# Optimization experiments

Measured on AMD Instinct MI355X. Metric: run time of the kernel, lower is better.

## Reference

```python
import jax, jax.numpy as jnp
import numpy as np

IN_F, OUT_F, RANK = 4096, 4096, 16
ALPHA = 32.0
SCALING = ALPHA / RANK


def setup_inputs() -> dict:
    key = jax.random.key(0)
    kx, kw, ka, kb = jax.random.split(key, 4)
    x = jax.random.normal(kx, (4, 2048, IN_F), dtype=jnp.float32)
    # base linear weight [out, in] (kaiming-uniform-like scale)
    bound_w = 1.0 / np.sqrt(IN_F)
    W = jax.random.uniform(kw, (OUT_F, IN_F), minval=-bound_w, maxval=bound_w, dtype=jnp.float32)
    # lora_A [rank, in]: kaiming uniform; lora_B [out, rank]: nonzero for testing
    bound_a = np.sqrt(6.0 / IN_F) / np.sqrt(1.0 + 5.0)
    lora_A = jax.random.uniform(ka, (RANK, IN_F), minval=-bound_a, maxval=bound_a, dtype=jnp.float32)
    lora_B = jax.random.normal(kb, (OUT_F, RANK), dtype=jnp.float32) * 0.02
    return {"x": x, "W": W, "lora_A": lora_A, "lora_B": lora_B}


def reference(x, W, lora_A, lora_B):
    # base: x @ W^T  -> [b, s, out]
    base = jnp.einsum("bsi,oi->bso", x, W)
    # low-rank path: (x @ A^T) @ B^T * scaling (dropout p=0 -> identity)
    r = jnp.einsum("bsi,ri->bsr", x, lora_A)  # [b, s, rank]
    lora = jnp.einsum("bsr,or->bso", r, lora_B) * SCALING
    return base + lora
```

## Files before the change

kernel.cpp:

```cpp
#include <hip/hip_runtime.h>
#include <stdint.h>
#include <stddef.h>

#define IN_F    4096
#define OUT_F   4096
#define MTOK    8192
#define RANK    16
#define SCALING 2.0f

typedef __attribute__((ext_vector_type(8))) short          bf16x8;
typedef __attribute__((ext_vector_type(4))) float          f32x4;
typedef __attribute__((ext_vector_type(4))) float          fl4;
typedef __attribute__((ext_vector_type(4))) unsigned short u16x4;
typedef __attribute__((ext_vector_type(8))) unsigned short u16x8;

static __device__ __forceinline__ unsigned short f2bf(float f) {
  union { float f; uint32_t u; } v; v.f = f;
  return (unsigned short)((v.u + 0x7fffu + ((v.u >> 16) & 1u)) >> 16);
}

static __device__ __forceinline__ void gload16(const void* g, void* l) {
  __builtin_amdgcn_global_load_lds(
      (const __attribute__((address_space(1))) uint32_t*)g,
      (__attribute__((address_space(3))) uint32_t*)l,
      16, 0, 0);
}

__global__ void merge_w_kernel(const float* __restrict__ W,
                               const float* __restrict__ lA,
                               const float* __restrict__ lB,
                               unsigned short* __restrict__ Weff) {
  __shared__ float Bs[RANK];
  const int o = blockIdx.x;
  if (threadIdx.x < RANK) Bs[threadIdx.x] = lB[o * RANK + threadIdx.x] * SCALING;
  __syncthreads();
  for (int c = threadIdx.x * 4; c < IN_F; c += 256 * 4) {
    fl4 w = *(const fl4*)(W + (size_t)o * IN_F + c);
#pragma unroll
    for (int r = 0; r < RANK; ++r) {
      const float b = Bs[r];
      const fl4 a = *(const fl4*)(lA + (size_t)r * IN_F + c);
      w[0] += b * a[0]; w[1] += b * a[1]; w[2] += b * a[2]; w[3] += b * a[3];
    }
    u16x4 p;
    p[0] = f2bf(w[0]); p[1] = f2bf(w[1]); p[2] = f2bf(w[2]); p[3] = f2bf(w[3]);
    *(u16x4*)(Weff + (size_t)o * IN_F + c) = p;
  }
}

__global__ void conv_x_kernel(const float* __restrict__ x,
                              unsigned short* __restrict__ xb) {
  const size_t i = ((size_t)blockIdx.x * 256 + threadIdx.x) * 8;
  const fl4 a = *(const fl4*)(x + i);
  const fl4 b = *(const fl4*)(x + i + 4);
  u16x8 p;
  p[0] = f2bf(a[0]); p[1] = f2bf(a[1]); p[2] = f2bf(a[2]); p[3] = f2bf(a[3]);
  p[4] = f2bf(b[0]); p[5] = f2bf(b[1]); p[6] = f2bf(b[2]); p[7] = f2bf(b[3]);
  *(u16x8*)(xb + i) = p;
}

__global__ __launch_bounds__(512, 2) void gemm8p_kernel(
    const unsigned short* __restrict__ X,
    const unsigned short* __restrict__ Wf,
    float* __restrict__ Out) {
  __shared__ char lds[131072];
  const int tid  = threadIdx.x;
  const int lane = tid & 63;
  const int wave = tid >> 6;
  const int wr = wave >> 2;
  const int wc = wave & 3;
  const int fr = lane & 15;
  const int fq = lane >> 4;

  const int bid = blockIdx.x;
  const int swz = (bid & 7) * 64 + (bid >> 3);
  const int tm = swz & 31;
  const int tn = swz >> 5;
  const int m0 = tm << 8;
  const int n0 = tn << 8;

  const unsigned short* Ag = X  + (size_t)m0 * IN_F;
  const unsigned short* Bg = Wf + (size_t)n0 * IN_F;

  const int rIW = lane >> 3;
  const int csw = ((lane & 7) ^ rIW) << 3;

  const int aBase = wr * 16384 + fr * 128;
  const int bBase = 65536 + (wc >> 1) * 16384 + (wc & 1) * 8192 + fr * 128;
  const int cA0 = (fq << 4) ^ ((fr & 7) << 4);
  const int cA1 = cA0 ^ 64;

#define STAGE(OP, H, BUF, K) do {                                              \
    const unsigned short* _g = (OP) ? Bg : Ag;                                 \
    const int _r0 = (H) * 128 + wave * 16 + rIW;                               \
    char* _d = lds + (OP) * 65536 + (BUF) * 32768 + (H) * 16384 +              \
               wave * 2048 + (lane << 4);                                      \
    gload16(_g + (size_t)_r0 * IN_F + (K) + csw, _d);                          \
    gload16(_g + (size_t)(_r0 + 8) * IN_F + (K) + csw, _d + 1024);             \
  } while (0)

#define LDA(BUF, M, KK) (*(const bf16x8*)(lds + (BUF) * 32768 + aBase + (M) * 2048 + (KK)))
#define LDB(BUF, N, KK) (*(const bf16x8*)(lds + (BUF) * 32768 + bBase + (N) * 2048 + (KK)))

  f32x4 acc[8][4];
#pragma unroll
  for (int i = 0; i < 8; ++i)
#pragma unroll
    for (int j = 0; j < 4; ++j) acc[i][j] = (f32x4){0.f, 0.f, 0.f, 0.f};

  bf16x8 a[8], b0[4], b1[4];

  STAGE(0, 0, 0, 0); STAGE(0, 1, 0, 0); STAGE(1, 0, 0, 0); STAGE(1, 1, 0, 0);

  for (int t = 0; t < 64; ++t) {
    const int b  = t & 1;
    const int nb = b ^ 1;
    const int kn = (t + 1) << 6;
    const bool pf = (t + 1 < 64);

    if (pf) {
      STAGE(0, 0, nb, kn);
      asm volatile("s_waitcnt vmcnt(2)" ::: "memory");
    } else {
      asm volatile("s_waitcnt vmcnt(0)" ::: "memory");
    }
    __builtin_amdgcn_s_barrier();
#pragma unroll
    for (int mi = 0; mi < 4; ++mi) { a[mi*2] = LDA(b, mi, cA0); a[mi*2+1] = LDA(b, mi, cA1); }
#pragma unroll
    for (int ni = 0; ni < 2; ++ni) { b0[ni*2] = LDB(b, ni, cA0); b0[ni*2+1] = LDB(b, ni, cA1); }
    asm volatile("s_waitcnt lgkmcnt(0)" ::: "memory");
    __builtin_amdgcn_s_setprio(1);
#pragma unroll
    for (int mi = 0; mi < 4; ++mi)
#pragma unroll
      for (int ni = 0; ni < 2; ++ni) {
        acc[mi][ni] = __builtin_amdgcn_mfma_f32_16x16x32_bf16(a[mi*2],   b0[ni*2],   acc[mi][ni], 0, 0, 0);
        acc[mi][ni] = __builtin_amdgcn_mfma_f32_16x16x32_bf16(a[mi*2+1], b0[ni*2+1], acc[mi][ni], 0, 0, 0);
      }
    __builtin_amdgcn_s_setprio(0);
    __builtin_amdgcn_s_barrier();

    if (pf) STAGE(0, 1, nb, kn);
    __builtin_amdgcn_s_barrier();
#pragma unroll
    for (int ni = 0; ni < 2; ++ni) { b1[ni*2] = LDB(b, 2+ni, cA0); b1[ni*2+1] = LDB(b, 2+ni, cA1); }
    asm volatile("s_waitcnt lgkmcnt(0)" ::: "memory");
    __builtin_amdgcn_s_setprio(1);
#pragma unroll
    for (int mi = 0; mi < 4; ++mi)
#pragma unroll
      for (int ni = 0; ni < 2; ++ni) {
        acc[mi][2+ni] = __builtin_amdgcn_mfma_f32_16x16x32_bf16(a[mi*2],   b1[ni*2],   acc[mi][2+ni], 0, 0, 0);
        acc[mi][2+ni] = __builtin_amdgcn_mfma_f32_16x16x32_bf16(a[mi*2+1], b1[ni*2+1], acc[mi][2+ni], 0, 0, 0);
      }
    __builtin_amdgcn_s_setprio(0);
    __builtin_amdgcn_s_barrier();

    if (pf) STAGE(1, 0, nb, kn);
    __builtin_amdgcn_s_barrier();
#pragma unroll
    for (int mi = 0; mi < 4; ++mi) { a[mi*2] = LDA(b, 4+mi, cA0); a[mi*2+1] = LDA(b, 4+mi, cA1); }
    asm volatile("s_waitcnt lgkmcnt(0)" ::: "memory");
    __builtin_amdgcn_s_setprio(1);
#pragma unroll
    for (int mi = 0; mi < 4; ++mi)
#pragma unroll
      for (int ni = 0; ni < 2; ++ni) {
        acc[4+mi][2+ni] = __builtin_amdgcn_mfma_f32_16x16x32_bf16(a[mi*2],   b1[ni*2],   acc[4+mi][2+ni], 0, 0, 0);
        acc[4+mi][2+ni] = __builtin_amdgcn_mfma_f32_16x16x32_bf16(a[mi*2+1], b1[ni*2+1], acc[4+mi][2+ni], 0, 0, 0);
      }
    __builtin_amdgcn_s_setprio(0);
    __builtin_amdgcn_s_barrier();

    if (pf) STAGE(1, 1, nb, kn);
    __builtin_amdgcn_s_barrier();
#pragma unroll
    for (int ni = 0; ni < 2; ++ni) { b0[ni*2] = LDB(b, ni, cA0); b0[ni*2+1] = LDB(b, ni, cA1); }
    asm volatile("s_waitcnt lgkmcnt(0)" ::: "memory");
    __builtin_amdgcn_s_setprio(1);
#pragma unroll
    for (int mi = 0; mi < 4; ++mi)
#pragma unroll
      for (int ni = 0; ni < 2; ++ni) {
        acc[4+mi][ni] = __builtin_amdgcn_mfma_f32_16x16x32_bf16(a[mi*2],   b0[ni*2],   acc[4+mi][ni], 0, 0, 0);
        acc[4+mi][ni] = __builtin_amdgcn_mfma_f32_16x16x32_bf16(a[mi*2+1], b0[ni*2+1], acc[4+mi][ni], 0, 0, 0);
      }
    __builtin_amdgcn_s_setprio(0);
    __builtin_amdgcn_s_barrier();
  }

#pragma unroll
  for (int mi = 0; mi < 8; ++mi) {
    const int row0 = m0 + wr * 128 + mi * 16 + fq * 4;
#pragma unroll
    for (int ni = 0; ni < 4; ++ni) {
      const int col = n0 + wc * 64 + ni * 16 + fr;
#pragma unroll
      for (int j = 0; j < 4; ++j)
        Out[(size_t)(row0 + j) * OUT_F + col] = acc[mi][ni][j];
    }
  }
#undef STAGE
#undef LDA
#undef LDB
}

__global__ __launch_bounds__(256) void gemm_f32x_kernel(
    const float* __restrict__ X,
    const unsigned short* __restrict__ Weff,
    float* __restrict__ Out) {
  __shared__ unsigned short As[128][32];
  __shared__ unsigned short Bs[128][32];

  const int tid  = threadIdx.x;
  const int lane = tid & 63;
  const int wave = tid >> 6;
  const int wr = wave >> 1, wc = wave & 1;
  const int fr = lane & 15, fq = lane >> 4;

  const int bid = blockIdx.x;
  const int m0 = (bid & 63) * 128;
  const int n0 = (bid >> 6) * 128;

  f32x4 acc[4][4];
#pragma unroll
  for (int i = 0; i < 4; ++i)
#pragma unroll
    for (int j = 0; j < 4; ++j) acc[i][j] = (f32x4){0.f, 0.f, 0.f, 0.f};

  const int srow = tid >> 2;
  const int sseg = tid & 3;

  for (int k0 = 0; k0 < IN_F; k0 += 32) {
    if (k0) __syncthreads();
    {
      const unsigned short* gB = Weff + (size_t)(n0 + srow) * IN_F + k0 + sseg * 8;
      gload16(gB, &Bs[srow][sseg * 8]);
      gload16(gB + (size_t)64 * IN_F, &Bs[64 + srow][sseg * 8]);
    }
#pragma unroll
    for (int it = 0; it < 4; ++it) {
      const int c   = tid + it * 256;
      const int row = c >> 3;
      const int c4  = (c & 7) * 4;
      const fl4 v = *(const fl4*)(X + (size_t)(m0 + row) * IN_F + k0 + c4);
      u16x4 p;
      p[0] = f2bf(v[0]); p[1] = f2bf(v[1]); p[2] = f2bf(v[2]); p[3] = f2bf(v[3]);
      *(u16x4*)&As[row][c4] = p;
    }
    __syncthreads();

    bf16x8 af[4], bfm[4];
#pragma unroll
    for (int m = 0; m < 4; ++m)
      af[m] = *(const bf16x8*)&As[wr * 64 + m * 16 + fr][fq * 8];
#pragma unroll
    for (int n = 0; n < 4; ++n)
      bfm[n] = *(const bf16x8*)&Bs[wc * 64 + n * 16 + fr][fq * 8];
#pragma unroll
    for (int m = 0; m < 4; ++m)
#pragma unroll
      for (int n = 0; n < 4; ++n)
        acc[m][n] = __builtin_amdgcn_mfma_f32_16x16x32_bf16(af[m], bfm[n], acc[m][n], 0, 0, 0);
  }

#pragma unroll
  for (int m = 0; m < 4; ++m) {
    const int row0 = m0 + wr * 64 + m * 16 + fq * 4;
#pragma unroll
    for (int n = 0; n < 4; ++n) {
      const int col = n0 + wc * 64 + n * 16 + fr;
#pragma unroll
      for (int j = 0; j < 4; ++j)
        Out[(size_t)(row0 + j) * OUT_F + col] = acc[m][n][j];
    }
  }
}

__global__ void lora_r_kernel(const float* __restrict__ x,
                              const float* __restrict__ lA,
                              float* __restrict__ r) {
  const int idx = blockIdx.x * 256 + threadIdx.x;
  const int m = idx / RANK, rr = idx % RANK;
  float acc = 0.f;
  for (int k = 0; k < IN_F; ++k)
    acc += x[(size_t)m * IN_F + k] * lA[(size_t)rr * IN_F + k];
  r[idx] = acc * SCALING;
}

__global__ void naive_out_kernel(const float* __restrict__ x,
                                 const float* __restrict__ W,
                                 const float* __restrict__ lB,
                                 const float* __restrict__ r,
                                 float* __restrict__ out) {
  const size_t idx = (size_t)blockIdx.x * 256 + threadIdx.x;
  const int m = (int)(idx / OUT_F), n = (int)(idx % OUT_F);
  float acc = 0.f;
  for (int k = 0; k < IN_F; ++k)
    acc += x[(size_t)m * IN_F + k] * W[(size_t)n * IN_F + k];
#pragma unroll
  for (int rr = 0; rr < RANK; ++rr)
    acc += r[(size_t)m * RANK + rr] * lB[(size_t)n * RANK + rr];
  out[idx] = acc;
}

extern "C" void kernel_launch(void* const* d_in, const int* in_sizes, int n_in,
                              void* d_out, int out_size, void* d_ws, size_t ws_size,
                              hipStream_t stream) {
  const float* x  = (const float*)d_in[0];
  const float* W  = (const float*)d_in[1];
  const float* lA = (const float*)d_in[2];
  const float* lB = (const float*)d_in[3];
  float* out = (float*)d_out;

  const size_t weff_bytes = (size_t)OUT_F * IN_F * 2;
  const size_t xb_bytes   = (size_t)MTOK * IN_F * 2;

  if (ws_size >= weff_bytes + xb_bytes) {
    unsigned short* Weff = (unsigned short*)d_ws;
    unsigned short* xb   = (unsigned short*)((char*)d_ws + weff_bytes);
    merge_w_kernel<<<OUT_F, 256, 0, stream>>>(W, lA, lB, Weff);
    conv_x_kernel<<<(MTOK * (size_t)IN_F) / (256 * 8), 256, 0, stream>>>(x, xb);
    gemm8p_kernel<<<(MTOK / 256) * (OUT_F / 256), 512, 0, stream>>>(xb, Weff, out);
  } else if (ws_size >= weff_bytes) {
    unsigned short* Weff = (unsigned short*)d_ws;
    merge_w_kernel<<<OUT_F, 256, 0, stream>>>(W, lA, lB, Weff);
    gemm_f32x_kernel<<<(MTOK / 128) * (OUT_F / 128), 256, 0, stream>>>(x, Weff, out);
  } else {
    float* r = (float*)d_ws;
    lora_r_kernel<<<(MTOK * RANK) / 256, 256, 0, stream>>>(x, lA, r);
    naive_out_kernel<<<(size_t)MTOK * OUT_F / 256, 256, 0, stream>>>(x, W, lB, r, out);
  }
}
```

Measured before the change: 364.0 us.

## Reorder staged loads so B tile lands first and overlap LDS reads with MFMA phases

Splits the global-to-LDS staging into separate A and B chunk macros and reorders the prefetch so B chunks are issued first and A chunks last. The vmcnt waits are relaxed to match. LDS fragment reads for the next MFMA phase are now issued before the barrier that follows the current phase, and the explicit lgkmcnt(0) waits are removed, so LDS reads overlap with MFMA execution. The intent is to cut barrier and wait stalls in the 256x256 bf16 GEMM main loop. The risk is that correctness now depends on the reworked wait counts, the buffer lifetimes and compiler-inserted lgkm waits.

```diff
diff --git a/kernel.cpp b/kernel.cpp
--- a/kernel.cpp
+++ b/kernel.cpp
@@ -90,13 +90,23 @@
   const int cA0 = (fq << 4) ^ ((fr & 7) << 4);
   const int cA1 = cA0 ^ 64;
 
-#define STAGE(OP, H, BUF, K) do {                                              \
-    const unsigned short* _g = (OP) ? Bg : Ag;                                 \
-    const int _r0 = (H) * 128 + wave * 16 + rIW;                               \
-    char* _d = lds + (OP) * 65536 + (BUF) * 32768 + (H) * 16384 +              \
-               wave * 2048 + (lane << 4);                                      \
-    gload16(_g + (size_t)_r0 * IN_F + (K) + csw, _d);                          \
-    gload16(_g + (size_t)(_r0 + 8) * IN_F + (K) + csw, _d + 1024);             \
+#define STAGE_A(C, BUF, K) do {                                                \
+    const int _rh = (C) * 64 + (wave & 3) * 16;                                \
+    const int _r0 = (wave >> 2) * 128 + _rh + rIW;                             \
+    char* _d = lds + (BUF) * 32768 + (wave >> 2) * 16384 + _rh * 128 +         \
+               (lane << 4);                                                    \
+    gload16(Ag + (size_t)_r0 * IN_F + (K) + csw, _d);                          \
+    gload16(Ag + (size_t)(_r0 + 8) * IN_F + (K) + csw, _d + 1024);             \
+  } while (0)
+
+#define STAGE_B(C, BUF, K) do {                                                \
+    const int _s  = wave >> 1;                                                 \
+    const int _rh = (_s & 1) * 64 + (C) * 32 + (wave & 1) * 16;                \
+    const int _r0 = (_s >> 1) * 128 + _rh + rIW;                               \
+    char* _d = lds + 65536 + (BUF) * 32768 + (_s >> 1) * 16384 + _rh * 128 +   \
+               (lane << 4);                                                    \
+    gload16(Bg + (size_t)_r0 * IN_F + (K) + csw, _d);                          \
+    gload16(Bg + (size_t)(_r0 + 8) * IN_F + (K) + csw, _d + 1024);             \
   } while (0)
 
 #define LDA(BUF, M, KK) (*(const bf16x8*)(lds + (BUF) * 32768 + aBase + (M) * 2048 + (KK)))
@@ -110,26 +120,25 @@
 
   bf16x8 a[8], b0[4], b1[4];
 
-  STAGE(0, 0, 0, 0); STAGE(0, 1, 0, 0); STAGE(1, 0, 0, 0); STAGE(1, 1, 0, 0);
+  STAGE_B(0, 0, 0); STAGE_B(1, 0, 0); STAGE_A(0, 0, 0); STAGE_A(1, 0, 0);
 
   for (int t = 0; t < 64; ++t) {
-    const int b  = t & 1;
-    const int nb = b ^ 1;
+    const int bu = t & 1;
+    const int nb = bu ^ 1;
     const int kn = (t + 1) << 6;
     const bool pf = (t + 1 < 64);
 
     if (pf) {
-      STAGE(0, 0, nb, kn);
+      STAGE_B(0, nb, kn);
+      asm volatile("s_waitcnt vmcnt(4)" ::: "memory");
+    } else {
       asm volatile("s_waitcnt vmcnt(2)" ::: "memory");
-    } else {
-      asm volatile("s_waitcnt vmcnt(0)" ::: "memory");
-    }
-    __builtin_amdgcn_s_barrier();
-#pragma unroll
-    for (int mi = 0; mi < 4; ++mi) { a[mi*2] = LDA(b, mi, cA0); a[mi*2+1] = LDA(b, mi, cA1); }
-#pragma unroll
-    for (int ni = 0; ni < 2; ++ni) { b0[ni*2] = LDB(b, ni, cA0); b0[ni*2+1] = LDB(b, ni, cA1); }
-    asm volatile("s_waitcnt lgkmcnt(0)" ::: "memory");
+    }
+    __builtin_amdgcn_s_barrier();
+#pragma unroll
+    for (int mi = 0; mi < 4; ++mi) { a[mi*2] = LDA(bu, mi, cA0); a[mi*2+1] = LDA(bu, mi, cA1); }
+#pragma unroll
+    for (int ni = 0; ni < 2; ++ni) { b0[ni*2] = LDB(bu, ni, cA0); b0[ni*2+1] = LDB(bu, ni, cA1); }
     __builtin_amdgcn_s_setprio(1);
 #pragma unroll
     for (int mi = 0; mi < 4; ++mi)
@@ -139,13 +148,17 @@
         acc[mi][ni] = __builtin_amdgcn_mfma_f32_16x16x32_bf16(a[mi*2+1], b0[ni*2+1], acc[mi][ni], 0, 0, 0);
       }
     __builtin_amdgcn_s_setprio(0);
-    __builtin_amdgcn_s_barrier();
-
-    if (pf) STAGE(0, 1, nb, kn);
-    __builtin_amdgcn_s_barrier();
-#pragma unroll
-    for (int ni = 0; ni < 2; ++ni) { b1[ni*2] = LDB(b, 2+ni, cA0); b1[ni*2+1] = LDB(b, 2+ni, cA1); }
-    asm volatile("s_waitcnt lgkmcnt(0)" ::: "memory");
+#pragma unroll
+    for (int ni = 0; ni < 2; ++ni) { b1[ni*2] = LDB(bu, 2+ni, cA0); b1[ni*2+1] = LDB(bu, 2+ni, cA1); }
+    __builtin_amdgcn_s_barrier();
+
+    if (pf) {
+      STAGE_B(1, nb, kn);
+      asm volatile("s_waitcnt vmcnt(4)" ::: "memory");
+    } else {
+      asm volatile("s_waitcnt vmcnt(0)" ::: "memory");
+    }
+    __builtin_amdgcn_s_barrier();
     __builtin_amdgcn_s_setprio(1);
 #pragma unroll
     for (int mi = 0; mi < 4; ++mi)
@@ -155,13 +168,12 @@
         acc[mi][2+ni] = __builtin_amdgcn_mfma_f32_16x16x32_bf16(a[mi*2+1], b1[ni*2+1], acc[mi][2+ni], 0, 0, 0);
       }
     __builtin_amdgcn_s_setprio(0);
-    __builtin_amdgcn_s_barrier();
-
-    if (pf) STAGE(1, 0, nb, kn);
-    __builtin_amdgcn_s_barrier();
-#pragma unroll
-    for (int mi = 0; mi < 4; ++mi) { a[mi*2] = LDA(b, 4+mi, cA0); a[mi*2+1] = LDA(b, 4+mi, cA1); }
-    asm volatile("s_waitcnt lgkmcnt(0)" ::: "memory");
+#pragma unroll
+    for (int mi = 0; mi < 4; ++mi) { a[mi*2] = LDA(bu, 4+mi, cA0); a[mi*2+1] = LDA(bu, 4+mi, cA1); }
+    __builtin_amdgcn_s_barrier();
+
+    if (pf) STAGE_A(0, nb, kn);
+    __builtin_amdgcn_s_barrier();
     __builtin_amdgcn_s_setprio(1);
 #pragma unroll
     for (int mi = 0; mi < 4; ++mi)
@@ -171,13 +183,12 @@
         acc[4+mi][2+ni] = __builtin_amdgcn_mfma_f32_16x16x32_bf16(a[mi*2+1], b1[ni*2+1], acc[4+mi][2+ni], 0, 0, 0);
       }
     __builtin_amdgcn_s_setprio(0);
-    __builtin_amdgcn_s_barrier();
-
-    if (pf) STAGE(1, 1, nb, kn);
-    __builtin_amdgcn_s_barrier();
-#pragma unroll
-    for (int ni = 0; ni < 2; ++ni) { b0[ni*2] = LDB(b, ni, cA0); b0[ni*2+1] = LDB(b, ni, cA1); }
-    asm volatile("s_waitcnt lgkmcnt(0)" ::: "memory");
+#pragma unroll
+    for (int ni = 0; ni < 2; ++ni) { b0[ni*2] = LDB(bu, ni, cA0); b0[ni*2+1] = LDB(bu, ni, cA1); }
+    __builtin_amdgcn_s_barrier();
+
+    if (pf) STAGE_A(1, nb, kn);
+    __builtin_amdgcn_s_barrier();
     __builtin_amdgcn_s_setprio(1);
 #pragma unroll
     for (int mi = 0; mi < 4; ++mi)
@@ -201,7 +212,8 @@
         Out[(size_t)(row0 + j) * OUT_F + col] = acc[mi][ni][j];
     }
   }
-#undef STAGE
+#undef STAGE_A
+#undef STAGE_B
 #undef LDA
 #undef LDB
 }
```

After: 340.9 us. 1.07x faster.

## Switch GEMM to 32x32x16 MFMA with MFMA-native LDS layout and fuse prep kernels

Applied to the files above, without the earlier changes.

Merges the weight-merge and x-conversion kernels into a single launch. Rewrites the main bf16 GEMM to use 32x32x16 MFMA instructions on f32x16 accumulators, which cuts the MFMA issue count. The global-to-LDS staging now writes tiles in the fragment order the instruction consumes, so no XOR swizzle is used. Next-slice LDS reads are issued before barriers so they overlap the current MFMAs, and the per-XCD tile mapping changes. The unswizzled layout risks LDS bank conflicts, and the larger accumulators raise register pressure.

```diff
diff --git a/kernel.cpp b/kernel.cpp
--- a/kernel.cpp
+++ b/kernel.cpp
@@ -8,11 +8,12 @@
 #define RANK    16
 #define SCALING 2.0f
 
-typedef __attribute__((ext_vector_type(8))) short          bf16x8;
-typedef __attribute__((ext_vector_type(4))) float          f32x4;
-typedef __attribute__((ext_vector_type(4))) float          fl4;
-typedef __attribute__((ext_vector_type(4))) unsigned short u16x4;
-typedef __attribute__((ext_vector_type(8))) unsigned short u16x8;
+typedef __attribute__((ext_vector_type(8)))  short          bf16x8;
+typedef __attribute__((ext_vector_type(4)))  float          f32x4;
+typedef __attribute__((ext_vector_type(16))) float          f32x16;
+typedef __attribute__((ext_vector_type(4)))  float          fl4;
+typedef __attribute__((ext_vector_type(4)))  unsigned short u16x4;
+typedef __attribute__((ext_vector_type(8)))  unsigned short u16x8;
 
 static __device__ __forceinline__ unsigned short f2bf(float f) {
   union { float f; uint32_t u; } v; v.f = f;
@@ -26,40 +27,41 @@
       16, 0, 0);
 }
 
-__global__ void merge_w_kernel(const float* __restrict__ W,
-                               const float* __restrict__ lA,
-                               const float* __restrict__ lB,
-                               unsigned short* __restrict__ Weff) {
+__global__ void prep_kernel(const float* __restrict__ x,
+                            const float* __restrict__ W,
+                            const float* __restrict__ lA,
+                            const float* __restrict__ lB,
+                            unsigned short* __restrict__ Weff,
+                            unsigned short* __restrict__ xb) {
   __shared__ float Bs[RANK];
-  const int o = blockIdx.x;
-  if (threadIdx.x < RANK) Bs[threadIdx.x] = lB[o * RANK + threadIdx.x] * SCALING;
-  __syncthreads();
-  for (int c = threadIdx.x * 4; c < IN_F; c += 256 * 4) {
-    fl4 w = *(const fl4*)(W + (size_t)o * IN_F + c);
-#pragma unroll
-    for (int r = 0; r < RANK; ++r) {
-      const float b = Bs[r];
-      const fl4 a = *(const fl4*)(lA + (size_t)r * IN_F + c);
-      w[0] += b * a[0]; w[1] += b * a[1]; w[2] += b * a[2]; w[3] += b * a[3];
-    }
-    u16x4 p;
-    p[0] = f2bf(w[0]); p[1] = f2bf(w[1]); p[2] = f2bf(w[2]); p[3] = f2bf(w[3]);
-    *(u16x4*)(Weff + (size_t)o * IN_F + c) = p;
-  }
-}
-
-__global__ void conv_x_kernel(const float* __restrict__ x,
-                              unsigned short* __restrict__ xb) {
-  const size_t i = ((size_t)blockIdx.x * 256 + threadIdx.x) * 8;
-  const fl4 a = *(const fl4*)(x + i);
-  const fl4 b = *(const fl4*)(x + i + 4);
-  u16x8 p;
-  p[0] = f2bf(a[0]); p[1] = f2bf(a[1]); p[2] = f2bf(a[2]); p[3] = f2bf(a[3]);
-  p[4] = f2bf(b[0]); p[5] = f2bf(b[1]); p[6] = f2bf(b[2]); p[7] = f2bf(b[3]);
-  *(u16x8*)(xb + i) = p;
-}
-
-__global__ __launch_bounds__(512, 2) void gemm8p_kernel(
+  if (blockIdx.x < OUT_F) {
+    const int o = blockIdx.x;
+    if (threadIdx.x < RANK) Bs[threadIdx.x] = lB[o * RANK + threadIdx.x] * SCALING;
+    __syncthreads();
+    for (int c = threadIdx.x * 4; c < IN_F; c += 256 * 4) {
+      fl4 w = *(const fl4*)(W + (size_t)o * IN_F + c);
+#pragma unroll
+      for (int r = 0; r < RANK; ++r) {
+        const float b = Bs[r];
+        const fl4 a = *(const fl4*)(lA + (size_t)r * IN_F + c);
+        w[0] += b * a[0]; w[1] += b * a[1]; w[2] += b * a[2]; w[3] += b * a[3];
+      }
+      u16x4 p;
+      p[0] = f2bf(w[0]); p[1] = f2bf(w[1]); p[2] = f2bf(w[2]); p[3] = f2bf(w[3]);
+      *(u16x4*)(Weff + (size_t)o * IN_F + c) = p;
+    }
+  } else {
+    const size_t i = ((size_t)(blockIdx.x - OUT_F) * 256 + threadIdx.x) * 8;
+    const fl4 a = *(const fl4*)(x + i);
+    const fl4 b = *(const fl4*)(x + i + 4);
+    u16x8 p;
+    p[0] = f2bf(a[0]); p[1] = f2bf(a[1]); p[2] = f2bf(a[2]); p[3] = f2bf(a[3]);
+    p[4] = f2bf(b[0]); p[5] = f2bf(b[1]); p[6] = f2bf(b[2]); p[7] = f2bf(b[3]);
+    *(u16x8*)(xb + i) = p;
+  }
+}
+
+__global__ __launch_bounds__(512, 2) void gemm32_kernel(
     const unsigned short* __restrict__ X,
     const unsigned short* __restrict__ Wf,
     float* __restrict__ Out) {
@@ -67,143 +69,123 @@
   const int tid  = threadIdx.x;
   const int lane = tid & 63;
   const int wave = tid >> 6;
-  const int wr = wave >> 2;
-  const int wc = wave & 3;
-  const int fr = lane & 15;
-  const int fq = lane >> 4;
-
-  const int bid = blockIdx.x;
-  const int swz = (bid & 7) * 64 + (bid >> 3);
-  const int tm = swz & 31;
-  const int tn = swz >> 5;
+  const int wr  = wave >> 2;
+  const int wc  = wave & 3;
+  const int l31 = lane & 31;
+  const int lhi = lane >> 5;
+
+  const int bid   = blockIdx.x;
+  const int xcd   = bid & 7;
+  const int local = bid >> 3;
+  const int tm = xcd * 4 + (local & 3);
+  const int tn = local >> 2;
   const int m0 = tm << 8;
   const int n0 = tn << 8;
 
   const unsigned short* Ag = X  + (size_t)m0 * IN_F;
   const unsigned short* Bg = Wf + (size_t)n0 * IN_F;
 
-  const int rIW = lane >> 3;
-  const int csw = ((lane & 7) ^ rIW) << 3;
-
-  const int aBase = wr * 16384 + fr * 128;
-  const int bBase = 65536 + (wc >> 1) * 16384 + (wc & 1) * 8192 + fr * 128;
-  const int cA0 = (fq << 4) ^ ((fr & 7) << 4);
-  const int cA1 = cA0 ^ 64;
-
-#define STAGE(OP, H, BUF, K) do {                                              \
-    const unsigned short* _g = (OP) ? Bg : Ag;                                 \
-    const int _r0 = (H) * 128 + wave * 16 + rIW;                               \
-    char* _d = lds + (OP) * 65536 + (BUF) * 32768 + (H) * 16384 +              \
-               wave * 2048 + (lane << 4);                                      \
-    gload16(_g + (size_t)_r0 * IN_F + (K) + csw, _d);                          \
-    gload16(_g + (size_t)(_r0 + 8) * IN_F + (K) + csw, _d + 1024);             \
+  const size_t srow = (size_t)(wave * 32 + l31) * IN_F;
+  const int    scol = lhi * 8;
+
+#define STAGE(KK, BUF, K0) do {                                                \
+    char* _dA = lds + (BUF) * 32768 + (KK) * 8192 + wave * 1024 + (lane << 4); \
+    gload16(Ag + srow + (K0) + (KK) * 16 + scol, _dA);                         \
+    gload16(Bg + srow + (K0) + (KK) * 16 + scol, _dA + 65536);                 \
   } while (0)
 
-#define LDA(BUF, M, KK) (*(const bf16x8*)(lds + (BUF) * 32768 + aBase + (M) * 2048 + (KK)))
-#define LDB(BUF, N, KK) (*(const bf16x8*)(lds + (BUF) * 32768 + bBase + (N) * 2048 + (KK)))
-
-  f32x4 acc[8][4];
-#pragma unroll
-  for (int i = 0; i < 8; ++i)
-#pragma unroll
-    for (int j = 0; j < 4; ++j) acc[i][j] = (f32x4){0.f, 0.f, 0.f, 0.f};
-
-  bf16x8 a[8], b0[4], b1[4];
-
-  STAGE(0, 0, 0, 0); STAGE(0, 1, 0, 0); STAGE(1, 0, 0, 0); STAGE(1, 1, 0, 0);
+#define LDA(BUF, MI, KK) (*(const bf16x8*)(lds + (BUF) * 32768 + (KK) * 8192 + (wr * 4 + (MI)) * 1024 + (lane << 4)))
+#define LDB(BUF, NI, KK) (*(const bf16x8*)(lds + 65536 + (BUF) * 32768 + (KK) * 8192 + (wc * 2 + (NI)) * 1024 + (lane << 4)))
+
+#define MFMA8(A, B)                                                            \
+  do {                                                                         \
+    _Pragma("unroll")                                                          \
+    for (int mi = 0; mi < 4; ++mi)                                             \
+      _Pragma("unroll")                                                        \
+      for (int ni = 0; ni < 2; ++ni)                                           \
+        acc[mi][ni] = __builtin_amdgcn_mfma_f32_32x32x16_bf16((A)[mi], (B)[ni], acc[mi][ni], 0, 0, 0); \
+  } while (0)
+
+  f32x16 acc[4][2];
+#pragma unroll
+  for (int i = 0; i < 4; ++i)
+#pragma unroll
+    for (int j = 0; j < 2; ++j)
+#pragma unroll
+      for (int e = 0; e < 16; ++e) acc[i][j][e] = 0.f;
+
+  bf16x8 a[4], b[2], a2[4], b2[2];
+
+  STAGE(0, 0, 0); STAGE(1, 0, 0); STAGE(2, 0, 0); STAGE(3, 0, 0);
 
   for (int t = 0; t < 64; ++t) {
-    const int b  = t & 1;
-    const int nb = b ^ 1;
+    const int bu = t & 1;
+    const int nb = bu ^ 1;
     const int kn = (t + 1) << 6;
     const bool pf = (t + 1 < 64);
 
     if (pf) {
-      STAGE(0, 0, nb, kn);
-      asm volatile("s_waitcnt vmcnt(2)" ::: "memory");
+      STAGE(0, nb, kn); STAGE(1, nb, kn);
+      asm volatile("s_waitcnt vmcnt(4)" ::: "memory");
     } else {
       asm volatile("s_waitcnt vmcnt(0)" ::: "memory");
     }
     __builtin_amdgcn_s_barrier();
 #pragma unroll
-    for (int mi = 0; mi < 4; ++mi) { a[mi*2] = LDA(b, mi, cA0); a[mi*2+1] = LDA(b, mi, cA1); }
-#pragma unroll
-    for (int ni = 0; ni < 2; ++ni) { b0[ni*2] = LDB(b, ni, cA0); b0[ni*2+1] = LDB(b, ni, cA1); }
-    asm volatile("s_waitcnt lgkmcnt(0)" ::: "memory");
+    for (int mi = 0; mi < 4; ++mi) a[mi] = LDA(bu, mi, 0);
+#pragma unroll
+    for (int ni = 0; ni < 2; ++ni) b[ni] = LDB(bu, ni, 0);
     __builtin_amdgcn_s_setprio(1);
-#pragma unroll
-    for (int mi = 0; mi < 4; ++mi)
-#pragma unroll
-      for (int ni = 0; ni < 2; ++ni) {
-        acc[mi][ni] = __builtin_amdgcn_mfma_f32_16x16x32_bf16(a[mi*2],   b0[ni*2],   acc[mi][ni], 0, 0, 0);
-        acc[mi][ni] = __builtin_amdgcn_mfma_f32_16x16x32_bf16(a[mi*2+1], b0[ni*2+1], acc[mi][ni], 0, 0, 0);
+    MFMA8(a, b);
+    __builtin_amdgcn_s_setprio(0);
+#pragma unroll
+    for (int mi = 0; mi < 4; ++mi) a2[mi] = LDA(bu, mi, 1);
+#pragma unroll
+    for (int ni = 0; ni < 2; ++ni) b2[ni] = LDB(bu, ni, 1);
+    __builtin_amdgcn_s_barrier();
+
+    if (pf) { STAGE(2, nb, kn); STAGE(3, nb, kn); }
+    __builtin_amdgcn_s_setprio(1);
+    MFMA8(a2, b2);
+    __builtin_amdgcn_s_setprio(0);
+#pragma unroll
+    for (int mi = 0; mi < 4; ++mi) a[mi] = LDA(bu, mi, 2);
+#pragma unroll
+    for (int ni = 0; ni < 2; ++ni) b[ni] = LDB(bu, ni, 2);
+    __builtin_amdgcn_s_barrier();
+
+    __builtin_amdgcn_s_setprio(1);
+    MFMA8(a, b);
+    __builtin_amdgcn_s_setprio(0);
+#pragma unroll
+    for (int mi = 0; mi < 4; ++mi) a2[mi] = LDA(bu, mi, 3);
+#pragma unroll
+    for (int ni = 0; ni < 2; ++ni) b2[ni] = LDB(bu, ni, 3);
+    __builtin_amdgcn_s_barrier();
+
+    __builtin_amdgcn_s_setprio(1);
+    MFMA8(a2, b2);
+    __builtin_amdgcn_s_setprio(0);
+    __builtin_amdgcn_s_barrier();
+  }
+
+#pragma unroll
+  for (int mi = 0; mi < 4; ++mi) {
+    const int rbase = m0 + wr * 128 + mi * 32 + lhi * 4;
+#pragma unroll
+    for (int ni = 0; ni < 2; ++ni) {
+      const int col = n0 + wc * 64 + ni * 32 + l31;
+#pragma unroll
+      for (int j = 0; j < 16; ++j) {
+        const int row = rbase + (j & 3) + 8 * (j >> 2);
+        Out[(size_t)row * OUT_F + col] = acc[mi][ni][j];
       }
-    __builtin_amdgcn_s_setprio(0);
-    __builtin_amdgcn_s_barrier();
-
-    if (pf) STAGE(0, 1, nb, kn);
-    __builtin_amdgcn_s_barrier();
-#pragma unroll
-    for (int ni = 0; ni < 2; ++ni) { b1[ni*2] = LDB(b, 2+ni, cA0); b1[ni*2+1] = LDB(b, 2+ni, cA1); }
-    asm volatile("s_waitcnt lgkmcnt(0)" ::: "memory");
-    __builtin_amdgcn_s_setprio(1);
-#pragma unroll
-    for (int mi = 0; mi < 4; ++mi)
-#pragma unroll
-      for (int ni = 0; ni < 2; ++ni) {
-        acc[mi][2+ni] = __builtin_amdgcn_mfma_f32_16x16x32_bf16(a[mi*2],   b1[ni*2],   acc[mi][2+ni], 0, 0, 0);
-        acc[mi][2+ni] = __builtin_amdgcn_mfma_f32_16x16x32_bf16(a[mi*2+1], b1[ni*2+1], acc[mi][2+ni], 0, 0, 0);
-      }
-    __builtin_amdgcn_s_setprio(0);
-    __builtin_amdgcn_s_barrier();
-
-    if (pf) STAGE(1, 0, nb, kn);
-    __builtin_amdgcn_s_barrier();
-#pragma unroll
-    for (int mi = 0; mi < 4; ++mi) { a[mi*2] = LDA(b, 4+mi, cA0); a[mi*2+1] = LDA(b, 4+mi, cA1); }
-    asm volatile("s_waitcnt lgkmcnt(0)" ::: "memory");
-    __builtin_amdgcn_s_setprio(1);
-#pragma unroll
-    for (int mi = 0; mi < 4; ++mi)
-#pragma unroll
-      for (int ni = 0; ni < 2; ++ni) {
-        acc[4+mi][2+ni] = __builtin_amdgcn_mfma_f32_16x16x32_bf16(a[mi*2],   b1[ni*2],   acc[4+mi][2+ni], 0, 0, 0);
-        acc[4+mi][2+ni] = __builtin_amdgcn_mfma_f32_16x16x32_bf16(a[mi*2+1], b1[ni*2+1], acc[4+mi][2+ni], 0, 0, 0);
-      }
-    __builtin_amdgcn_s_setprio(0);
-    __builtin_amdgcn_s_barrier();
-
-    if (pf) STAGE(1, 1, nb, kn);
-    __builtin_amdgcn_s_barrier();
-#pragma unroll
-    for (int ni = 0; ni < 2; ++ni) { b0[ni*2] = LDB(b, ni, cA0); b0[ni*2+1] = LDB(b, ni, cA1); }
-    asm volatile("s_waitcnt lgkmcnt(0)" ::: "memory");
-    __builtin_amdgcn_s_setprio(1);
-#pragma unroll
-    for (int mi = 0; mi < 4; ++mi)
-#pragma unroll
-      for (int ni = 0; ni < 2; ++ni) {
-        acc[4+mi][ni] = __builtin_amdgcn_mfma_f32_16x16x32_bf16(a[mi*2],   b0[ni*2],   acc[4+mi][ni], 0, 0, 0);
-        acc[4+mi][ni] = __builtin_amdgcn_mfma_f32_16x16x32_bf16(a[mi*2+1], b0[ni*2+1], acc[4+mi][ni], 0, 0, 0);
-      }
-    __builtin_amdgcn_s_setprio(0);
-    __builtin_amdgcn_s_barrier();
-  }
-
-#pragma unroll
-  for (int mi = 0; mi < 8; ++mi) {
-    const int row0 = m0 + wr * 128 + mi * 16 + fq * 4;
-#pragma unroll
-    for (int ni = 0; ni < 4; ++ni) {
-      const int col = n0 + wc * 64 + ni * 16 + fr;
-#pragma unroll
-      for (int j = 0; j < 4; ++j)
-        Out[(size_t)(row0 + j) * OUT_F + col] = acc[mi][ni][j];
     }
   }
 #undef STAGE
 #undef LDA
 #undef LDB
+#undef MFMA8
 }
 
 __global__ __launch_bounds__(256) void gemm_f32x_kernel(
@@ -320,12 +302,12 @@
   if (ws_size >= weff_bytes + xb_bytes) {
     unsigned short* Weff = (unsigned short*)d_ws;
     unsigned short* xb   = (unsigned short*)((char*)d_ws + weff_bytes);
-    merge_w_kernel<<<OUT_F, 256, 0, stream>>>(W, lA, lB, Weff);
-    conv_x_kernel<<<(MTOK * (size_t)IN_F) / (256 * 8), 256, 0, stream>>>(x, xb);
-    gemm8p_kernel<<<(MTOK / 256) * (OUT_F / 256), 512, 0, stream>>>(xb, Weff, out);
+    const int conv_blocks = (int)((MTOK * (size_t)IN_F) / (256 * 8));
+    prep_kernel<<<OUT_F + conv_blocks, 256, 0, stream>>>(x, W, lA, lB, Weff, xb);
+    gemm32_kernel<<<(MTOK / 256) * (OUT_F / 256), 512, 0, stream>>>(xb, Weff, out);
   } else if (ws_size >= weff_bytes) {
     unsigned short* Weff = (unsigned short*)d_ws;
-    merge_w_kernel<<<OUT_F, 256, 0, stream>>>(W, lA, lB, Weff);
+    prep_kernel<<<OUT_F, 256, 0, stream>>>(x, W, lA, lB, Weff, (unsigned short*)0);
     gemm_f32x_kernel<<<(MTOK / 128) * (OUT_F / 128), 256, 0, stream>>>(x, Weff, out);
   } else {
     float* r = (float*)d_ws;
```

After: 407.8 us. 1.12x slower.
